# Optimization experiments

Measured on AMD Instinct MI355X. Metric: run time of the kernel, lower is better.

Reference implementation:

```python
import jax, jax.numpy as jnp
import numpy as np

E = 1024   # embed_dim
H = 16     # num_heads
NQ = 8     # ffn_dim == n_qubits
B, S = 2, 2048


def setup_inputs() -> dict:
    key = jax.random.key(0)
    ks = jax.random.split(key, 8)
    g = lambda k, sh, sc=1.0: jax.random.normal(k, sh, jnp.float32) * sc
    return {
        "x": g(ks[0], (B, S, E)),
        "w_qkv": g(ks[1], (3 * E, E), 0.02),      # nn.Linear(E, 3E, bias=False).weight
        "w_comb": g(ks[2], (E, E), 0.02),          # combine Linear weight
        "b_comb": jnp.zeros((E,), jnp.float32),
        "gamma1": jnp.ones((E,), jnp.float32),     # norm1
        "beta1": jnp.zeros((E,), jnp.float32),
        "gamma2": jnp.ones((E,), jnp.float32),     # norm2
        "beta2": jnp.zeros((E,), jnp.float32),
        "theta": g(ks[3], (NQ,)),                  # trainable RY angles
        "w1": g(ks[4], (1, NQ), 0.3),              # linear1 weight [1, n_qubits]
        "b1": jnp.zeros((1,), jnp.float32),
    }


def _layernorm(x, g, b, eps=1e-5):
    m = jnp.mean(x, axis=-1, keepdims=True)
    v = jnp.var(x, axis=-1, keepdims=True)
    return (x - m) * jax.lax.rsqrt(v + eps) * g + b


def reference(x, w_qkv, w_comb, b_comb, gamma1, beta1, gamma2, beta2, theta, w1, b1):
    Bx, Sx, Em = x.shape
    dk = Em // H
    # ---- attention ----
    qkv = (x @ w_qkv.T).reshape(Bx, Sx, 3, H, dk)
    q = jnp.transpose(qkv[:, :, 0], (0, 2, 1, 3))  # [B,H,S,dk]
    k = jnp.transpose(qkv[:, :, 1], (0, 2, 1, 3))
    v = jnp.transpose(qkv[:, :, 2], (0, 2, 1, 3))
    scores = jnp.einsum('bhqd,bhkd->bhqk', q, k) / jnp.sqrt(jnp.float32(dk))
    probs = jax.nn.softmax(scores, axis=-1)        # dropout = identity (eval)
    out = jnp.einsum('bhqk,bhkd->bhqd', probs, v)
    out = jnp.transpose(out, (0, 2, 1, 3)).reshape(Bx, Sx, Em)
    attn = out @ w_comb.T + b_comb
    x1 = _layernorm(x + attn, gamma1, beta1)
    # ---- quantum FFN: RX(x_i) encode, RY(theta_i), <Z_i> = cos(theta_i)*cos(x_i) ----
    z = jnp.cos(x1[..., :theta.shape[0]]) * jnp.cos(theta)  # [B,S,NQ]
    ffn = z @ w1.T + b1                                      # [B,S,1], broadcasts
    return _layernorm(x1 + ffn, gamma2, beta2)
```

## Files before the change

### kernel.cpp

```cpp
#include <hip/hip_runtime.h>
#include <hip/hip_bf16.h>
#include <math.h>

typedef __bf16 bf16;
typedef bf16 bf16x8 __attribute__((ext_vector_type(8)));
typedef bf16 bf16x4 __attribute__((ext_vector_type(4)));
typedef float f32x4 __attribute__((ext_vector_type(4)));
typedef unsigned int u32;

#define EMB 1024
#define NH 16
#define DK 64
#define SEQ 2048
#define NB 2
#define NTOK (NB*SEQ)

#define QSCALE 0.18033688011112043f

#if defined(__has_builtin)
#if __has_builtin(__builtin_amdgcn_exp2f)
#define EXP2(x) __builtin_amdgcn_exp2f(x)
#else
#define EXP2(x) exp2f(x)
#endif
#else
#define EXP2(x) exp2f(x)
#endif

__device__ __forceinline__ void gl_lds16(const void* g, void* l) {
    __builtin_amdgcn_global_load_lds(
        (const __attribute__((address_space(1))) u32*)g,
        (__attribute__((address_space(3))) u32*)l, 16, 0, 0);
}

#define SWZ(row, colblk) (((row)*64) + ((((colblk) ^ ((row)&7)))*8))

#define PSTR 72

__device__ __forceinline__ void xcd_remap(int gx, int* bx, int* by) {
    int gy  = gridDim.y;
    int nwg = gx * gy;
    int wg  = *by * gx + *bx;
    int per = nwg >> 3;
    int s   = (wg & 7) * per + (wg >> 3);
    *bx = s % gx;
    *by = s / gx;
}

__global__ __launch_bounds__(256) void convert3(
    const float* __restrict__ s0, const float* __restrict__ s1,
    const float* __restrict__ s2,
    bf16* __restrict__ d0, bf16* __restrict__ d1, bf16* __restrict__ d2)
{
    const float* src; bf16* dst; int n;
    switch (blockIdx.y) {
        case 0:  src = s0; dst = d0; n = NTOK*EMB;  break;
        case 1:  src = s1; dst = d1; n = 3*EMB*EMB; break;
        default: src = s2; dst = d2; n = EMB*EMB;   break;
    }
    int i = (blockIdx.x * 256 + threadIdx.x) * 4;
    if (i + 3 < n) {
        float4 v = *(const float4*)(src + i);
        dst[i+0] = (bf16)v.x; dst[i+1] = (bf16)v.y;
        dst[i+2] = (bf16)v.z; dst[i+3] = (bf16)v.w;
    }
}

template<int MODE, int BM>
__global__ __launch_bounds__(256) void gemm_bt(
    const bf16* __restrict__ Aa, const bf16* __restrict__ Bb,
    bf16* __restrict__ qb, bf16* __restrict__ kb, bf16* __restrict__ vtb,
    float* __restrict__ outc, int Kdim)
{
    constexpr int MI = BM / 32;
    __shared__ __align__(16) bf16 At[BM*64];
    __shared__ __align__(16) bf16 Bt[128*64];
    const int tid  = threadIdx.x;
    const int w    = tid >> 6, lane = tid & 63;
    const int quad = lane >> 4, l15 = lane & 15;
    const int wr   = w >> 1,   wc  = w & 1;
    int bx = blockIdx.x, by = blockIdx.y;
    xcd_remap(gridDim.x, &bx, &by);
    const int m0 = by * BM, n0 = bx * 128;
    const int lrow = lane >> 3;
    const int lswz = ((lane & 7) ^ lrow) * 8;

    f32x4 acc[MI][4] = {};

    for (int k0 = 0; k0 < Kdim; k0 += 64) {
        __syncthreads();
        for (int i = 0; i < MI; ++i) {
            int r = w*(BM/4) + i*8 + lrow;
            gl_lds16(Aa + (size_t)(m0 + r)*Kdim + k0 + lswz, At + (w*(BM/4) + i*8)*64);
        }
        for (int i = 0; i < 4; ++i) {
            int r = w*32 + i*8 + lrow;
            gl_lds16(Bb + (size_t)(n0 + r)*Kdim + k0 + lswz, Bt + (w*32 + i*8)*64);
        }
        __syncthreads();
        for (int kk = 0; kk < 2; ++kk) {
            bf16x8 a[MI], b[4];
            for (int i = 0; i < MI; ++i) {
                int row = wr*(BM/2) + i*16 + l15;
                a[i] = *(const bf16x8*)(At + SWZ(row, 4*kk + quad));
            }
            for (int j = 0; j < 4; ++j) {
                int row = wc*64 + j*16 + l15;
                b[j] = *(const bf16x8*)(Bt + SWZ(row, 4*kk + quad));
            }
            __builtin_amdgcn_s_setprio(1);
            for (int i = 0; i < MI; ++i)
                for (int j = 0; j < 4; ++j)
                    acc[i][j] = __builtin_amdgcn_mfma_f32_16x16x32_bf16(a[i], b[j], acc[i][j], 0, 0, 0);
            __builtin_amdgcn_s_setprio(0);
        }
    }

    for (int i = 0; i < MI; ++i) for (int j = 0; j < 4; ++j) {
        int rb  = m0 + wr*(BM/2) + i*16 + quad*4;
        int col = n0 + wc*64 + j*16 + l15;
        if (MODE == 0) {
            int c = col >> 10, h = (col >> 6) & 15, d = col & 63;
            int b_ = rb >> 11, s = rb & 2047;
            int bh = b_*NH + h;
            if (c == 2) {
                bf16 tmp[4] __attribute__((aligned(8)));
                for (int r = 0; r < 4; ++r) tmp[r] = (bf16)acc[i][j][r];
                *(ushort4*)(vtb + ((size_t)bh*DK + d)*SEQ + s) = *(ushort4*)tmp;
            } else if (c == 0) {
                for (int r = 0; r < 4; ++r)
                    qb[((size_t)bh*SEQ + s + r)*DK + d] = (bf16)(acc[i][j][r] * QSCALE);
            } else {
                for (int r = 0; r < 4; ++r)
                    kb[((size_t)bh*SEQ + s + r)*DK + d] = (bf16)acc[i][j][r];
            }
        } else {
            for (int r = 0; r < 4; ++r)
                outc[(size_t)(rb + r)*EMB + col] = acc[i][j][r];
        }
    }
}

__global__ __launch_bounds__(512) void attn_kernel(
    const bf16* __restrict__ q, const bf16* __restrict__ k,
    const bf16* __restrict__ vt, bf16* __restrict__ out)
{
    __shared__ __align__(16) bf16 QP[8*16*PSTR];
    __shared__ __align__(16) bf16 Kt0[64*64];
    __shared__ __align__(16) bf16 Kt1[64*64];
    __shared__ __align__(16) bf16 Vt0[64*64];
    __shared__ __align__(16) bf16 Vt1[64*64];

    const int tid  = threadIdx.x;
    const int w    = tid >> 6, lane = tid & 63;
    const int quad = lane >> 4, l15 = lane & 15;
    int qt = blockIdx.x, bh = blockIdx.y;
    xcd_remap(gridDim.x, &qt, &bh);
    const int lrow = lane >> 3;
    const int lswz = ((lane & 7) ^ lrow) * 8;

    for (int i = 0; i < 2; ++i) {
        int r = w*16 + i*8 + lrow;
        gl_lds16(q + ((size_t)bh*SEQ + qt*128 + r)*DK + lswz, QP + (w*16 + i*8)*64);
    }
    asm volatile("s_waitcnt vmcnt(0)" ::: "memory");

    bf16x8 qf[2];
    for (int kk = 0; kk < 2; ++kk)
        qf[kk] = *(const bf16x8*)(QP + SWZ(w*16 + l15, 4*kk + quad));

    bf16* Pw = QP + w * 16 * PSTR;

    f32x4 O[4] = {};
    float psum = 0.f;

    auto stage_kv = [&](int kt, bf16* Kb, bf16* Vb) {
        int r = w*8 + lrow;
        gl_lds16(k  + ((size_t)bh*SEQ + kt*64 + r)*DK + lswz, Kb + (w*8)*64);
        gl_lds16(vt + ((size_t)bh*DK + r)*SEQ + kt*64 + lswz, Vb + (w*8)*64);
    };

    auto compute = [&](const bf16* Kb, const bf16* Vb) {
        f32x4 sc[4] = {};
        for (int kk = 0; kk < 2; ++kk) {
            bf16x8 kf[4];
            for (int j = 0; j < 4; ++j)
                kf[j] = *(const bf16x8*)(Kb + SWZ(j*16 + l15, 4*kk + quad));
            __builtin_amdgcn_s_setprio(1);
            for (int j = 0; j < 4; ++j)
                sc[j] = __builtin_amdgcn_mfma_f32_16x16x32_bf16(kf[j], qf[kk], sc[j], 0, 0, 0);
            __builtin_amdgcn_s_setprio(0);
        }
        for (int j = 0; j < 4; ++j) {
            bf16x4 pk;
            for (int r = 0; r < 4; ++r) {
                float p = EXP2(sc[j][r]);
                psum += p;
                pk[r] = (bf16)p;
            }
            *(bf16x4*)(Pw + l15*PSTR + j*16 + quad*4) = pk;
        }
        asm volatile("s_waitcnt lgkmcnt(0)" ::: "memory");
        for (int kk = 0; kk < 2; ++kk) {
            bf16x8 vb[4];
            for (int j = 0; j < 4; ++j)
                vb[j] = *(const bf16x8*)(Vb + SWZ(j*16 + l15, 4*kk + quad));
            bf16x8 a = *(const bf16x8*)(Pw + l15*PSTR + kk*32 + quad*8);
            __builtin_amdgcn_s_setprio(1);
            for (int j = 0; j < 4; ++j)
                O[j] = __builtin_amdgcn_mfma_f32_16x16x32_bf16(a, vb[j], O[j], 0, 0, 0);
            __builtin_amdgcn_s_setprio(0);
        }
    };

    stage_kv(0, Kt0, Vt0);
    for (int kt2 = 0; kt2 < SEQ/128; ++kt2) {
        __syncthreads();
        stage_kv(2*kt2 + 1, Kt1, Vt1);
        compute(Kt0, Vt0);
        __syncthreads();
        if (kt2 + 1 < SEQ/128)
            stage_kv(2*kt2 + 2, Kt0, Vt0);
        compute(Kt1, Vt1);
    }

    float s = psum;
    s += __shfl_xor(s, 16, 64);
    s += __shfl_xor(s, 32, 64);
    float inv[4];
    for (int r = 0; r < 4; ++r)
        inv[r] = 1.f / __shfl(s, quad*4 + r, 64);

    const int b_ = bh >> 4, h = bh & 15;
    for (int j = 0; j < 4; ++j)
        for (int r = 0; r < 4; ++r) {
            int t   = b_*SEQ + qt*128 + w*16 + quad*4 + r;
            int col = h*DK + j*16 + l15;
            out[(size_t)t*EMB + col] = (bf16)(O[j][r] * inv[r]);
        }
}

__global__ __launch_bounds__(256) void ln_kernel(
    const float* __restrict__ x, const float* __restrict__ comb,
    const float* __restrict__ bcomb,
    const float* __restrict__ g1, const float* __restrict__ be1,
    const float* __restrict__ g2, const float* __restrict__ be2,
    const float* __restrict__ theta, const float* __restrict__ w1v,
    const float* __restrict__ b1v, float* __restrict__ out)
{
    const int t = blockIdx.x, tid = threadIdx.x;
    __shared__ float red[8];
    __shared__ float fp2[2];
    const int e0 = tid*4;

    float4 xv = *(const float4*)(x    + (size_t)t*EMB + e0);
    float4 cv = *(const float4*)(comb + (size_t)t*EMB + e0);
    float4 bv = *(const float4*)(bcomb + e0);
    float r[4] = { xv.x + cv.x + bv.x, xv.y + cv.y + bv.y,
                   xv.z + cv.z + bv.z, xv.w + cv.w + bv.w };

    float s = 0.f, ss = 0.f;
    for (int i = 0; i < 4; ++i) { s += r[i]; ss += r[i]*r[i]; }
    for (int m = 1; m < 64; m <<= 1) { s += __shfl_xor(s, m, 64); ss += __shfl_xor(ss, m, 64); }
    if ((tid & 63) == 0) { red[(tid>>6)*2] = s; red[(tid>>6)*2+1] = ss; }
    __syncthreads();
    s  = red[0] + red[2] + red[4] + red[6];
    ss = red[1] + red[3] + red[5] + red[7];
    float mean = s * (1.f/1024.f);
    float var  = ss * (1.f/1024.f) - mean*mean;
    float inv  = rsqrtf(var + 1e-5f);
    float x1[4];
    for (int i = 0; i < 4; ++i) {
        int e = e0 + i;
        x1[i] = (r[i] - mean)*inv*g1[e] + be1[e];
    }
    __syncthreads();
    if (e0 < 8) {
        float pf = 0.f;
        for (int i = 0; i < 4; ++i) {
            int e = e0 + i;
            pf += cosf(x1[i]) * cosf(theta[e]) * w1v[e];
        }
        fp2[tid] = pf;
    }
    __syncthreads();
    float f = fp2[0] + fp2[1] + b1v[0];

    float s2 = 0.f, ss2 = 0.f;
    for (int i = 0; i < 4; ++i) { float v2 = x1[i] + f; s2 += v2; ss2 += v2*v2; }
    for (int m = 1; m < 64; m <<= 1) { s2 += __shfl_xor(s2, m, 64); ss2 += __shfl_xor(ss2, m, 64); }
    if ((tid & 63) == 0) { red[(tid>>6)*2] = s2; red[(tid>>6)*2+1] = ss2; }
    __syncthreads();
    s2  = red[0] + red[2] + red[4] + red[6];
    ss2 = red[1] + red[3] + red[5] + red[7];
    float mean2 = s2 * (1.f/1024.f);
    float var2  = ss2 * (1.f/1024.f) - mean2*mean2;
    float inv2  = rsqrtf(var2 + 1e-5f);
    float4 ov;
    ov.x = ((x1[0] + f) - mean2)*inv2*g2[e0+0] + be2[e0+0];
    ov.y = ((x1[1] + f) - mean2)*inv2*g2[e0+1] + be2[e0+1];
    ov.z = ((x1[2] + f) - mean2)*inv2*g2[e0+2] + be2[e0+2];
    ov.w = ((x1[3] + f) - mean2)*inv2*g2[e0+3] + be2[e0+3];
    *(float4*)(out + (size_t)t*EMB + e0) = ov;
}

extern "C" void kernel_launch(void* const* d_in, const int* in_sizes, int n_in,
                              void* d_out, int out_size, void* d_ws, size_t ws_size,
                              hipStream_t stream)
{
    const float* x      = (const float*)d_in[0];
    const float* w_qkv  = (const float*)d_in[1];
    const float* w_comb = (const float*)d_in[2];
    const float* b_comb = (const float*)d_in[3];
    const float* g1     = (const float*)d_in[4];
    const float* be1    = (const float*)d_in[5];
    const float* g2     = (const float*)d_in[6];
    const float* be2    = (const float*)d_in[7];
    const float* theta  = (const float*)d_in[8];
    const float* w1v    = (const float*)d_in[9];
    const float* b1v    = (const float*)d_in[10];
    float* out = (float*)d_out;

    char* ws = (char*)d_ws;
    bf16*  xb     = (bf16*)(ws);
    bf16*  wqkvb  = (bf16*)(ws + ( 8u<<20));
    bf16*  wcombb = (bf16*)(ws + (14u<<20));
    bf16*  qb     = (bf16*)(ws + (16u<<20));
    bf16*  kb     = (bf16*)(ws + (24u<<20));
    bf16*  vtb    = (bf16*)(ws + (32u<<20));
    bf16*  attn   = (bf16*)(ws + (40u<<20));
    float* comb   = (float*)(ws + (16u<<20));

    convert3<<<dim3(4096, 3), 256, 0, stream>>>(x, w_qkv, w_comb, xb, wqkvb, wcombb);

    gemm_bt<0,128><<<dim3(3*EMB/128, NTOK/128), 256, 0, stream>>>(
        xb, wqkvb, qb, kb, vtb, nullptr, EMB);
    attn_kernel<<<dim3(SEQ/128, NB*NH), 512, 0, stream>>>(qb, kb, vtb, attn);
    gemm_bt<1,64><<<dim3(EMB/128, NTOK/64), 256, 0, stream>>>(
        attn, wcombb, nullptr, nullptr, nullptr, comb, EMB);
    ln_kernel<<<NTOK, 256, 0, stream>>>(x, comb, b_comb, g1, be1, g2, be2,
                                        theta, w1v, b1v, out);
}
```

Baseline: 202.4 us.

## Warp-specialize attention: QK/softmax waves and PV waves pipelined via shared P buffers

The attention kernel splits its 8 waves into two roles. Four waves compute QK^T scores and exp for a 64-key tile, each covering a 64-query by 32-key block, and write P into a double-buffered shared array. The other four waves issue the K/V global-to-LDS loads and run the PV MFMA one tile behind, using a triple-buffered V. Row sums are combined through shared memory at the end, and launch bounds now request 4 waves per SIMD. This aims to overlap the exp/softmax work with the PV matrix multiply, at the cost of more LDS and a per-tile block barrier.

```diff
diff --git a/kernel.cpp b/kernel.cpp
--- a/kernel.cpp
+++ b/kernel.cpp
@@ -141,15 +141,18 @@
     }
 }
 
-__global__ __launch_bounds__(512) void attn_kernel(
+__global__ __launch_bounds__(512, 4) void attn_kernel(
     const bf16* __restrict__ q, const bf16* __restrict__ k,
     const bf16* __restrict__ vt, bf16* __restrict__ out)
 {
-    __shared__ __align__(16) bf16 QP[8*16*PSTR];
+    __shared__ __align__(16) bf16 Pa[128*PSTR];
+    __shared__ __align__(16) bf16 Pb[128*PSTR];
     __shared__ __align__(16) bf16 Kt0[64*64];
     __shared__ __align__(16) bf16 Kt1[64*64];
     __shared__ __align__(16) bf16 Vt0[64*64];
     __shared__ __align__(16) bf16 Vt1[64*64];
+    __shared__ __align__(16) bf16 Vt2[64*64];
+    __shared__ float PS[2][128];
 
     const int tid  = threadIdx.x;
     const int w    = tid >> 6, lane = tid & 63;
@@ -158,86 +161,135 @@
     xcd_remap(gridDim.x, &qt, &bh);
     const int lrow = lane >> 3;
     const int lswz = ((lane & 7) ^ lrow) * 8;
-
+    const int NT = SEQ / 64;
+
+    const int kh = w & 1, qh = w >> 1;
+    const int v4 = w - 4;
+
+    #pragma unroll
     for (int i = 0; i < 2; ++i) {
         int r = w*16 + i*8 + lrow;
-        gl_lds16(q + ((size_t)bh*SEQ + qt*128 + r)*DK + lswz, QP + (w*16 + i*8)*64);
+        gl_lds16(q + ((size_t)bh*SEQ + qt*128 + r)*DK + lswz, Pa + (w*16 + i*8)*64);
+    }
+    if (w >= 4) {
+        #pragma unroll
+        for (int i = 0; i < 2; ++i) {
+            int r = v4*16 + i*8 + lrow;
+            gl_lds16(k  + ((size_t)bh*SEQ + r)*DK + lswz, Kt0 + (v4*16 + i*8)*64);
+            gl_lds16(vt + ((size_t)bh*DK + r)*SEQ + lswz, Vt0 + (v4*16 + i*8)*64);
+        }
     }
     asm volatile("s_waitcnt vmcnt(0)" ::: "memory");
-
-    bf16x8 qf[2];
-    for (int kk = 0; kk < 2; ++kk)
-        qf[kk] = *(const bf16x8*)(QP + SWZ(w*16 + l15, 4*kk + quad));
-
-    bf16* Pw = QP + w * 16 * PSTR;
-
-    f32x4 O[4] = {};
-    float psum = 0.f;
-
-    auto stage_kv = [&](int kt, bf16* Kb, bf16* Vb) {
-        int r = w*8 + lrow;
-        gl_lds16(k  + ((size_t)bh*SEQ + kt*64 + r)*DK + lswz, Kb + (w*8)*64);
-        gl_lds16(vt + ((size_t)bh*DK + r)*SEQ + kt*64 + lswz, Vb + (w*8)*64);
-    };
-
-    auto compute = [&](const bf16* Kb, const bf16* Vb) {
-        f32x4 sc[4] = {};
-        for (int kk = 0; kk < 2; ++kk) {
-            bf16x8 kf[4];
-            for (int j = 0; j < 4; ++j)
-                kf[j] = *(const bf16x8*)(Kb + SWZ(j*16 + l15, 4*kk + quad));
-            __builtin_amdgcn_s_setprio(1);
-            for (int j = 0; j < 4; ++j)
-                sc[j] = __builtin_amdgcn_mfma_f32_16x16x32_bf16(kf[j], qf[kk], sc[j], 0, 0, 0);
-            __builtin_amdgcn_s_setprio(0);
-        }
-        for (int j = 0; j < 4; ++j) {
-            bf16x4 pk;
+    __syncthreads();
+
+    bf16x8 qf[4][2];
+    if (w < 4) {
+        #pragma unroll
+        for (int t = 0; t < 4; ++t)
+            #pragma unroll
+            for (int kk = 0; kk < 2; ++kk)
+                qf[t][kk] = *(const bf16x8*)(Pa + SWZ(qh*64 + t*16 + l15, 4*kk + quad));
+    }
+
+    f32x4 O[2][4] = {};
+    float psum[4] = {};
+
+    for (int it = 0; it <= NT; ++it) {
+        __syncthreads();
+        if (w >= 4) {
+            if (it + 1 < NT) {
+                bf16* Kn = ((it+1) & 1) ? Kt1 : Kt0;
+                int vmn = (it+1) % 3;
+                bf16* Vn = (vmn == 0) ? Vt0 : (vmn == 1) ? Vt1 : Vt2;
+                #pragma unroll
+                for (int i = 0; i < 2; ++i) {
+                    int r = v4*16 + i*8 + lrow;
+                    gl_lds16(k  + ((size_t)bh*SEQ + (it+1)*64 + r)*DK + lswz, Kn + (v4*16 + i*8)*64);
+                    gl_lds16(vt + ((size_t)bh*DK + r)*SEQ + (it+1)*64 + lswz, Vn + (v4*16 + i*8)*64);
+                }
+            }
+            if (it > 0) {
+                int pt = it - 1;
+                const bf16* Pr = (pt & 1) ? Pb : Pa;
+                int vmr = pt % 3;
+                const bf16* Vb = (vmr == 0) ? Vt0 : (vmr == 1) ? Vt1 : Vt2;
+                #pragma unroll
+                for (int kk = 0; kk < 2; ++kk) {
+                    bf16x8 vb[4];
+                    #pragma unroll
+                    for (int j = 0; j < 4; ++j)
+                        vb[j] = *(const bf16x8*)(Vb + SWZ(j*16 + l15, 4*kk + quad));
+                    bf16x8 a0 = *(const bf16x8*)(Pr + (v4*32 +  0 + l15)*PSTR + kk*32 + quad*8);
+                    bf16x8 a1 = *(const bf16x8*)(Pr + (v4*32 + 16 + l15)*PSTR + kk*32 + quad*8);
+                    __builtin_amdgcn_s_setprio(1);
+                    #pragma unroll
+                    for (int j = 0; j < 4; ++j) {
+                        O[0][j] = __builtin_amdgcn_mfma_f32_16x16x32_bf16(a0, vb[j], O[0][j], 0, 0, 0);
+                        O[1][j] = __builtin_amdgcn_mfma_f32_16x16x32_bf16(a1, vb[j], O[1][j], 0, 0, 0);
+                    }
+                    __builtin_amdgcn_s_setprio(0);
+                }
+            }
+        } else if (it < NT) {
+            const bf16* Kb = (it & 1) ? Kt1 : Kt0;
+            bf16* Pw = (it & 1) ? Pb : Pa;
+            f32x4 sc[2][4] = {};
+            #pragma unroll
+            for (int kk = 0; kk < 2; ++kk) {
+                bf16x8 kf0 = *(const bf16x8*)(Kb + SWZ(kh*32 +  0 + l15, 4*kk + quad));
+                bf16x8 kf1 = *(const bf16x8*)(Kb + SWZ(kh*32 + 16 + l15, 4*kk + quad));
+                __builtin_amdgcn_s_setprio(1);
+                #pragma unroll
+                for (int t = 0; t < 4; ++t) {
+                    sc[0][t] = __builtin_amdgcn_mfma_f32_16x16x32_bf16(kf0, qf[t][kk], sc[0][t], 0, 0, 0);
+                    sc[1][t] = __builtin_amdgcn_mfma_f32_16x16x32_bf16(kf1, qf[t][kk], sc[1][t], 0, 0, 0);
+                }
+                __builtin_amdgcn_s_setprio(0);
+            }
+            #pragma unroll
+            for (int s = 0; s < 2; ++s)
+                #pragma unroll
+                for (int t = 0; t < 4; ++t) {
+                    bf16x4 pk;
+                    #pragma unroll
+                    for (int r = 0; r < 4; ++r) {
+                        float p = EXP2(sc[s][t][r]);
+                        psum[t] += p;
+                        pk[r] = (bf16)p;
+                    }
+                    *(bf16x4*)(Pw + (qh*64 + t*16 + l15)*PSTR + kh*32 + s*16 + quad*4) = pk;
+                }
+        }
+    }
+
+    if (w < 4) {
+        #pragma unroll
+        for (int t = 0; t < 4; ++t) {
+            float s = psum[t];
+            s += __shfl_xor(s, 16, 64);
+            s += __shfl_xor(s, 32, 64);
+            if (lane < 16)
+                PS[kh][qh*64 + t*16 + lane] = s;
+        }
+    }
+    __syncthreads();
+
+    if (w >= 4) {
+        const int b_ = bh >> 4, h = bh & 15;
+        #pragma unroll
+        for (int st = 0; st < 2; ++st)
+            #pragma unroll
             for (int r = 0; r < 4; ++r) {
-                float p = EXP2(sc[j][r]);
-                psum += p;
-                pk[r] = (bf16)p;
-            }
-            *(bf16x4*)(Pw + l15*PSTR + j*16 + quad*4) = pk;
-        }
-        asm volatile("s_waitcnt lgkmcnt(0)" ::: "memory");
-        for (int kk = 0; kk < 2; ++kk) {
-            bf16x8 vb[4];
-            for (int j = 0; j < 4; ++j)
-                vb[j] = *(const bf16x8*)(Vb + SWZ(j*16 + l15, 4*kk + quad));
-            bf16x8 a = *(const bf16x8*)(Pw + l15*PSTR + kk*32 + quad*8);
-            __builtin_amdgcn_s_setprio(1);
-            for (int j = 0; j < 4; ++j)
-                O[j] = __builtin_amdgcn_mfma_f32_16x16x32_bf16(a, vb[j], O[j], 0, 0, 0);
-            __builtin_amdgcn_s_setprio(0);
-        }
-    };
-
-    stage_kv(0, Kt0, Vt0);
-    for (int kt2 = 0; kt2 < SEQ/128; ++kt2) {
-        __syncthreads();
-        stage_kv(2*kt2 + 1, Kt1, Vt1);
-        compute(Kt0, Vt0);
-        __syncthreads();
-        if (kt2 + 1 < SEQ/128)
-            stage_kv(2*kt2 + 2, Kt0, Vt0);
-        compute(Kt1, Vt1);
-    }
-
-    float s = psum;
-    s += __shfl_xor(s, 16, 64);
-    s += __shfl_xor(s, 32, 64);
-    float inv[4];
-    for (int r = 0; r < 4; ++r)
-        inv[r] = 1.f / __shfl(s, quad*4 + r, 64);
-
-    const int b_ = bh >> 4, h = bh & 15;
-    for (int j = 0; j < 4; ++j)
-        for (int r = 0; r < 4; ++r) {
-            int t   = b_*SEQ + qt*128 + w*16 + quad*4 + r;
-            int col = h*DK + j*16 + l15;
-            out[(size_t)t*EMB + col] = (bf16)(O[j][r] * inv[r]);
-        }
+                int qrow = v4*32 + st*16 + quad*4 + r;
+                float inv = 1.f / (PS[0][qrow] + PS[1][qrow]);
+                #pragma unroll
+                for (int j = 0; j < 4; ++j) {
+                    int t_  = b_*SEQ + qt*128 + qrow;
+                    int col = h*DK + j*16 + l15;
+                    out[(size_t)t_*EMB + col] = (bf16)(O[st][j][r] * inv);
+                }
+            }
+    }
 }
 
 __global__ __launch_bounds__(256) void ln_kernel(
```

Measured after the change: 208.0 us. +2.8%, slower.
